# Kernel tuning notes

Hardware: AMD Instinct MI355X
Metric: run time of the kernel (lower is better)

Reference implementation:

```python
import jax, jax.numpy as jnp
import numpy as np

N, C_IN, C_OUT, H, W = 16, 256, 256, 32, 32
K = 9  # 3x3 kernel


def setup_inputs() -> dict:
    key = jax.random.key(0)
    k1, k2, k3 = jax.random.split(key, 3)
    x = jax.random.normal(k1, (N, C_IN, H, W), dtype=jnp.float32)
    # offsets as produced upstream from anchors: (N, H*W, 18)
    offset = jax.random.normal(k2, (N, H * W, 2 * K), dtype=jnp.float32)
    # DeformConv weight (no bias), kaiming-ish scale
    weight = jax.random.normal(k3, (C_OUT, C_IN, 3, 3), dtype=jnp.float32) * 0.02
    return {"x": x, "offset": offset, "weight": weight}


def _deform_conv3x3(x, offset_nchw, weight):
    """DeformConv v1, kernel 3x3, stride 1, padding 1, dilation 1,
    groups=1, deformable_groups=1, zero padding outside borders."""
    n, c, h, w = x.shape
    o = weight.shape[0]
    # offset channel layout: (dy_k, dx_k) pairs for k = 0..8
    off = offset_nchw.reshape(n, K, 2, h, w)
    dy = off[:, :, 0]  # (N,K,H,W)
    dx = off[:, :, 1]
    ky = (jnp.arange(K) // 3 - 1).astype(x.dtype)  # kernel row offsets -1,0,1
    kx = (jnp.arange(K) % 3 - 1).astype(x.dtype)
    base_y = jnp.arange(h, dtype=x.dtype)[None, None, :, None]
    base_x = jnp.arange(w, dtype=x.dtype)[None, None, None, :]
    py = base_y + ky[None, :, None, None] + dy  # (N,K,H,W) sample rows
    px = base_x + kx[None, :, None, None] + dx  # (N,K,H,W) sample cols

    y0 = jnp.floor(py)
    x0 = jnp.floor(px)
    ly = py - y0  # fractional parts
    lx = px - x0

    x_flat = x.reshape(n, c, h * w)

    def corner(yi, xi, wgt):
        valid = (yi >= 0) & (yi <= h - 1) & (xi >= 0) & (xi <= w - 1)
        yc = jnp.clip(yi, 0, h - 1).astype(jnp.int32)
        xc = jnp.clip(xi, 0, w - 1).astype(jnp.int32)
        idx = (yc * w + xc).reshape(n, K * h * w)
        g = jax.vmap(lambda xf, i: xf[:, i])(x_flat, idx)  # (N,C,K*H*W)
        wv = (wgt * valid.astype(x.dtype)).reshape(n, 1, K * h * w)
        return g * wv

    val = (corner(y0, x0, (1 - ly) * (1 - lx))
           + corner(y0, x0 + 1, (1 - ly) * lx)
           + corner(y0 + 1, x0, ly * (1 - lx))
           + corner(y0 + 1, x0 + 1, ly * lx))
    val = val.reshape(n, c, K, h, w)  # sampled im2col columns
    return jnp.einsum('nckhw,ock->nohw', val, weight.reshape(o, c, K))


def reference(x, offset, weight):
    n, _, h, w = x.shape
    assert h * w == offset.shape[1]
    # AdaptiveConv.forward: (N, HW, 18) -> (N, 18, H, W)
    offset_nchw = jnp.transpose(offset, (0, 2, 1)).reshape(n, 2 * K, h, w)
    return _deform_conv3x3(x, offset_nchw, weight)
```

## Files before the change

kernel.cpp:

```cpp
#include <hip/hip_runtime.h>

#define NB   16
#define CIN  256
#define COUT 256
#define HH   32
#define WW   32
#define HW   1024
#define KK   9
#define CK   2304

typedef __bf16 bf16x8 __attribute__((ext_vector_type(8)));
typedef float  f32x4  __attribute__((ext_vector_type(4)));

__device__ __forceinline__ unsigned short f2bf(float f) {
    unsigned int u = __float_as_uint(f);
    u += 0x7FFFu + ((u >> 16) & 1u);
    return (unsigned short)(u >> 16);
}
__device__ __forceinline__ float bfhi(unsigned int u) {
    return __uint_as_float(u & 0xFFFF0000u);
}
__device__ __forceinline__ float bflo(unsigned int u) {
    return __uint_as_float(u << 16);
}

typedef const __attribute__((address_space(1))) void* gas_ptr;
typedef __attribute__((address_space(3))) void* las_ptr;

__device__ __forceinline__ void async16(const void* g, void* l) {
    __builtin_amdgcn_global_load_lds((gas_ptr)g, (las_ptr)l, 16, 0, 0);
}

__global__ __launch_bounds__(256) void wconv_kernel(const float* __restrict__ w,
                                                    unsigned short* __restrict__ wbf) {
    __shared__ float ls[CK];
    const int o = blockIdx.x;
    const float* wo = w + (size_t)o * CK;
#pragma unroll
    for (int i = threadIdx.x; i < CK; i += 256) ls[i] = wo[i];
    __syncthreads();
    unsigned short* dst = wbf + (size_t)o * CK;
#pragma unroll
    for (int i = threadIdx.x; i < CK; i += 256) {
        int k = i >> 8, c = i & 255;
        dst[i] = f2bf(ls[c * KK + k]);
    }
}

__global__ __launch_bounds__(256) void xt_kernel(const float* __restrict__ x,
                                                 unsigned short* __restrict__ xtb) {
    __shared__ float ls[64][65];
    const int c0  = blockIdx.x * 64;
    const int hw0 = blockIdx.y * 64;
    const int n   = blockIdx.z;
    const int t   = threadIdx.x;
    {
        int c = t >> 2, q = t & 3;
        const float4* base = (const float4*)(x + ((size_t)(n * CIN + c0 + c)) * HW + hw0 + q * 16);
#pragma unroll
        for (int j = 0; j < 4; ++j) {
            float4 v = base[j];
            ls[c][q * 16 + j * 4 + 0] = v.x;
            ls[c][q * 16 + j * 4 + 1] = v.y;
            ls[c][q * 16 + j * 4 + 2] = v.z;
            ls[c][q * 16 + j * 4 + 3] = v.w;
        }
    }
    __syncthreads();
    {
        int hw = t >> 2, seg = (t & 3) * 16;
        unsigned int dw[8];
#pragma unroll
        for (int j = 0; j < 8; ++j) {
            float f0 = ls[seg + 2 * j][hw];
            float f1 = ls[seg + 2 * j + 1][hw];
            dw[j] = (unsigned)f2bf(f0) | ((unsigned)f2bf(f1) << 16);
        }
        uint4* dst = (uint4*)(xtb + ((size_t)(n * HW + hw0 + hw)) * CIN + c0 + seg);
        dst[0] = *(uint4*)&dw[0];
        dst[1] = *(uint4*)&dw[4];
    }
}

__global__ __launch_bounds__(512, 2) void fused_kernel(const unsigned short* __restrict__ wbf,
                                                       const unsigned short* __restrict__ xtb,
                                                       const float* __restrict__ off,
                                                       float* __restrict__ out) {
    __shared__ unsigned short As[2][256 * 64];
    __shared__ unsigned short Bs[2][64 * 64];

    const int tid  = threadIdx.x;
    const int wv   = tid >> 6;
    const int lane = tid & 63;
    const int quad = lane >> 4;
    const int l15  = lane & 15;

    const int hw_local = tid >> 3;
    const int seg      = tid & 7;

    const int id  = blockIdx.x;
    const int n   = ((id & 7) << 1) | ((id >> 3) & 1);
    const int hw0 = (id >> 4) * 64;

    const int hw = hw0 + hw_local;
    const int h  = hw >> 5, w = hw & 31;

    const int srow   = lane >> 3;
    const int schunk = (lane & 7) ^ (srow & 7);

    const uint4*  xb4  = (const uint4*)(xtb + (size_t)n * HW * CIN);
    const float2* offp = (const float2*)(off + ((size_t)n * HW + hw) * (2 * KK));

    f32x4 acc[2][4] = {};

    auto setup = [&](int tap, float wg[4], int ix[4]) {
        float2 o = offp[tap];
        float py = (float)(h + tap / 3 - 1) + o.x;
        float px = (float)(w + tap % 3 - 1) + o.y;
        float y0f = floorf(py), x0f = floorf(px);
        float ly = py - y0f, lx = px - x0f;
        int y0 = (int)y0f, x0 = (int)x0f;
#pragma unroll
        for (int c2 = 0; c2 < 4; ++c2) {
            int yy = y0 + (c2 >> 1);
            int xx = x0 + (c2 & 1);
            float wy = (c2 >> 1) ? ly : 1.0f - ly;
            float wx = (c2 & 1) ? lx : 1.0f - lx;
            bool v = (yy >= 0) && (yy < HH) && (xx >= 0) && (xx < WW);
            wg[c2] = v ? wy * wx : 0.0f;
            int yc = yy < 0 ? 0 : (yy > HH - 1 ? HH - 1 : yy);
            int xc = xx < 0 ? 0 : (xx > WW - 1 ? WW - 1 : xx);
            ix[c2] = yc * WW + xc;
        }
    };

    auto loadc = [&](uint4 cr[4], const int ix[4], int s) {
#pragma unroll
        for (int c2 = 0; c2 < 4; ++c2)
            cr[c2] = xb4[(size_t)ix[c2] * 32 + s * 8 + seg];
    };

    auto build = [&](int nb, int ckb, const uint4 cr[4], const float wg[4]) {
#pragma unroll
        for (int j = 0; j < 4; ++j) {
            int rb = wv * 32 + j * 8;
            async16(wbf + (size_t)(rb + srow) * CK + ckb + schunk * 8, &As[nb][rb * 64]);
        }
        unsigned u0[4], u1[4], u2[4], u3[4];
        *(uint4*)u0 = cr[0]; *(uint4*)u1 = cr[1];
        *(uint4*)u2 = cr[2]; *(uint4*)u3 = cr[3];
        unsigned dw[4];
#pragma unroll
        for (int d = 0; d < 4; ++d) {
            float lo = wg[0] * bflo(u0[d]) + wg[1] * bflo(u1[d])
                     + wg[2] * bflo(u2[d]) + wg[3] * bflo(u3[d]);
            float hi = wg[0] * bfhi(u0[d]) + wg[1] * bfhi(u1[d])
                     + wg[2] * bfhi(u2[d]) + wg[3] * bfhi(u3[d]);
            dw[d] = (unsigned)f2bf(lo) | ((unsigned)f2bf(hi) << 16);
        }
        *(uint4*)&Bs[nb][hw_local * 64 + (seg ^ (hw_local & 7)) * 8] = *(uint4*)dw;
    };

    auto mfma_step = [&](int pb) {
        bf16x8 af[2][2], bfr[4][2];
#pragma unroll
        for (int mi = 0; mi < 2; ++mi)
#pragma unroll
            for (int hh = 0; hh < 2; ++hh) {
                int row = wv * 32 + mi * 16 + l15;
                int ch  = (hh * 4 + quad) ^ (row & 7);
                af[mi][hh] = *(const bf16x8*)&As[pb][row * 64 + ch * 8];
            }
#pragma unroll
        for (int ni = 0; ni < 4; ++ni)
#pragma unroll
            for (int hh = 0; hh < 2; ++hh) {
                int row = ni * 16 + l15;
                int ch  = (hh * 4 + quad) ^ (row & 7);
                bfr[ni][hh] = *(const bf16x8*)&Bs[pb][row * 64 + ch * 8];
            }
#pragma unroll
        for (int mi = 0; mi < 2; ++mi)
#pragma unroll
            for (int ni = 0; ni < 4; ++ni) {
                acc[mi][ni] = __builtin_amdgcn_mfma_f32_16x16x32_bf16(af[mi][0], bfr[ni][0], acc[mi][ni], 0, 0, 0);
                acc[mi][ni] = __builtin_amdgcn_mfma_f32_16x16x32_bf16(af[mi][1], bfr[ni][1], acc[mi][ni], 0, 0, 0);
            }
    };

    float wgc[4], wgn[4];
    int   ixc[4], ixn[4];
    uint4 crA[4], crB[4];

    setup(0, wgc, ixc);
    loadc(crA, ixc, 0);
    build(0, 0, crA, wgc);
    loadc(crB, ixc, 1);
    __syncthreads();

    for (int tap = 0; tap < 9; ++tap) {
        const int ckb = tap * 256;
        build(1, ckb + 64, crB, wgc);
        loadc(crA, ixc, 2);
        mfma_step(0);
        __syncthreads();
        build(0, ckb + 128, crA, wgc);
        loadc(crB, ixc, 3);
        mfma_step(1);
        __syncthreads();
        build(1, ckb + 192, crB, wgc);
        if (tap < 8) { setup(tap + 1, wgn, ixn); loadc(crA, ixn, 0); }
        mfma_step(0);
        __syncthreads();
        if (tap < 8) {
            build(0, ckb + 256, crA, wgn);
            loadc(crB, ixn, 1);
#pragma unroll
            for (int c2 = 0; c2 < 4; ++c2) { wgc[c2] = wgn[c2]; ixc[c2] = ixn[c2]; }
            mfma_step(1);
            __syncthreads();
        } else {
            mfma_step(1);
        }
    }

    float* opnt = out + (size_t)n * COUT * HW + hw0;
#pragma unroll
    for (int mi = 0; mi < 2; ++mi)
#pragma unroll
        for (int ni = 0; ni < 4; ++ni) {
            int col = ni * 16 + l15;
#pragma unroll
            for (int rr = 0; rr < 4; ++rr) {
                int row = wv * 32 + mi * 16 + quad * 4 + rr;
                opnt[(size_t)row * HW + col] = acc[mi][ni][rr];
            }
        }
}

extern "C" void kernel_launch(void* const* d_in, const int* in_sizes, int n_in,
                              void* d_out, int out_size, void* d_ws, size_t ws_size,
                              hipStream_t stream) {
    const float* x   = (const float*)d_in[0];
    const float* off = (const float*)d_in[1];
    const float* wt  = (const float*)d_in[2];
    float* out = (float*)d_out;

    unsigned short* wbf = (unsigned short*)d_ws;
    unsigned short* xtb = (unsigned short*)((char*)d_ws + 1179648);

    wconv_kernel<<<256, 256, 0, stream>>>(wt, wbf);
    xt_kernel<<<dim3(4, 16, 16), 256, 0, stream>>>(x, xtb);
    fused_kernel<<<256, 512, 0, stream>>>(wbf, xtb, off, out);
}
```

Measured before the change: 122.3 us.

## Triple-buffer weight tiles with async LDS DMA and manual barrier scheduling

The weight (A) tile buffer goes from double to triple buffering, so each async global-to-LDS weight copy is issued two k-steps ahead instead of one. The original __syncthreads is replaced by a manual lgkmcnt wait plus s_barrier wrapped in sched_barriers, with explicit sched_barrier fences placed between the DMA, lerp, gather-load and MFMA phases. s_setprio is raised around the MFMA block. The aim is to hide weight-load latency and stop the compiler from reordering or over-waiting on memory. The third A buffer adds 32KB of LDS and the main loop is no longer unrolled. Waiting only on lgkmcnt could also let the async LDS loads (vmcnt) go unfinished before they are read.

Measured after the change: 122.1 us. About the same (-0.1%).

```diff
diff --git a/kernel.cpp b/kernel.cpp
--- a/kernel.cpp
+++ b/kernel.cpp
@@ -30,6 +30,10 @@
 __device__ __forceinline__ void async16(const void* g, void* l) {
     __builtin_amdgcn_global_load_lds((gas_ptr)g, (las_ptr)l, 16, 0, 0);
 }
+
+#define SB() __builtin_amdgcn_sched_barrier(0)
+#define SYNC() do { SB(); asm volatile("s_waitcnt lgkmcnt(0)" ::: "memory"); SB(); \
+                    __builtin_amdgcn_s_barrier(); SB(); } while (0)
 
 __global__ __launch_bounds__(256) void wconv_kernel(const float* __restrict__ w,
                                                     unsigned short* __restrict__ wbf) {
@@ -86,7 +90,7 @@
                                                        const unsigned short* __restrict__ xtb,
                                                        const float* __restrict__ off,
                                                        float* __restrict__ out) {
-    __shared__ unsigned short As[2][256 * 64];
+    __shared__ unsigned short As[3][256 * 64];
     __shared__ unsigned short Bs[2][64 * 64];
 
     const int tid  = threadIdx.x;
@@ -113,10 +117,9 @@
 
     f32x4 acc[2][4] = {};
 
-    auto setup = [&](int tap, float wg[4], int ix[4]) {
-        float2 o = offp[tap];
-        float py = (float)(h + tap / 3 - 1) + o.x;
-        float px = (float)(w + tap % 3 - 1) + o.y;
+    auto setup2 = [&](float2 o, int tapv, float* wg, int* ix) {
+        float py = (float)(h + tapv / 3 - 1) + o.x;
+        float px = (float)(w + tapv % 3 - 1) + o.y;
         float y0f = floorf(py), x0f = floorf(px);
         float ly = py - y0f, lx = px - x0f;
         int y0 = (int)y0f, x0 = (int)x0f;
@@ -134,18 +137,23 @@
         }
     };
 
-    auto loadc = [&](uint4 cr[4], const int ix[4], int s) {
+    auto loadc = [&](uint4 cr[4], const int* ix, int q) {
 #pragma unroll
         for (int c2 = 0; c2 < 4; ++c2)
-            cr[c2] = xb4[(size_t)ix[c2] * 32 + s * 8 + seg];
-    };
-
-    auto build = [&](int nb, int ckb, const uint4 cr[4], const float wg[4]) {
+            cr[c2] = xb4[(size_t)ix[c2] * 32 + q * 8 + seg];
+    };
+
+    auto dmaA = [&](int ai, int kblk) {
+        const unsigned short* wsrc = wbf + (size_t)kblk * 64 + (size_t)srow * CK + schunk * 8;
+        unsigned short* dst = &As[ai][0];
 #pragma unroll
         for (int j = 0; j < 4; ++j) {
             int rb = wv * 32 + j * 8;
-            async16(wbf + (size_t)(rb + srow) * CK + ckb + schunk * 8, &As[nb][rb * 64]);
-        }
+            async16(wsrc + (size_t)rb * CK, dst + rb * 64);
+        }
+    };
+
+    auto lerpB = [&](int bi, const uint4 cr[4], const float* wg) {
         unsigned u0[4], u1[4], u2[4], u3[4];
         *(uint4*)u0 = cr[0]; *(uint4*)u1 = cr[1];
         *(uint4*)u2 = cr[2]; *(uint4*)u3 = cr[3];
@@ -158,10 +166,12 @@
                      + wg[2] * bfhi(u2[d]) + wg[3] * bfhi(u3[d]);
             dw[d] = (unsigned)f2bf(lo) | ((unsigned)f2bf(hi) << 16);
         }
-        *(uint4*)&Bs[nb][hw_local * 64 + (seg ^ (hw_local & 7)) * 8] = *(uint4*)dw;
-    };
-
-    auto mfma_step = [&](int pb) {
+        *(uint4*)&Bs[bi][hw_local * 64 + (seg ^ (hw_local & 7)) * 8] = *(uint4*)dw;
+    };
+
+    auto mfma_step = [&](int ai, int bi) {
+        const unsigned short* Ap = &As[ai][0];
+        const unsigned short* Bp = &Bs[bi][0];
         bf16x8 af[2][2], bfr[4][2];
 #pragma unroll
         for (int mi = 0; mi < 2; ++mi)
@@ -169,7 +179,7 @@
             for (int hh = 0; hh < 2; ++hh) {
                 int row = wv * 32 + mi * 16 + l15;
                 int ch  = (hh * 4 + quad) ^ (row & 7);
-                af[mi][hh] = *(const bf16x8*)&As[pb][row * 64 + ch * 8];
+                af[mi][hh] = *(const bf16x8*)(Ap + row * 64 + ch * 8);
             }
 #pragma unroll
         for (int ni = 0; ni < 4; ++ni)
@@ -177,8 +187,9 @@
             for (int hh = 0; hh < 2; ++hh) {
                 int row = ni * 16 + l15;
                 int ch  = (hh * 4 + quad) ^ (row & 7);
-                bfr[ni][hh] = *(const bf16x8*)&Bs[pb][row * 64 + ch * 8];
+                bfr[ni][hh] = *(const bf16x8*)(Bp + row * 64 + ch * 8);
             }
+        __builtin_amdgcn_s_setprio(1);
 #pragma unroll
         for (int mi = 0; mi < 2; ++mi)
 #pragma unroll
@@ -186,42 +197,78 @@
                 acc[mi][ni] = __builtin_amdgcn_mfma_f32_16x16x32_bf16(af[mi][0], bfr[ni][0], acc[mi][ni], 0, 0, 0);
                 acc[mi][ni] = __builtin_amdgcn_mfma_f32_16x16x32_bf16(af[mi][1], bfr[ni][1], acc[mi][ni], 0, 0, 0);
             }
+        __builtin_amdgcn_s_setprio(0);
     };
 
     float wgc[4], wgn[4];
     int   ixc[4], ixn[4];
     uint4 crA[4], crB[4];
-
-    setup(0, wgc, ixc);
-    loadc(crA, ixc, 0);
-    build(0, 0, crA, wgc);
-    loadc(crB, ixc, 1);
-    __syncthreads();
-
+    {
+        float2 o0 = offp[0];
+        setup2(o0, 0, wgc, ixc);
+        dmaA(0, 0);
+        dmaA(1, 1);
+        SB();
+        loadc(crA, ixc, 0);
+        loadc(crB, ixc, 1);
+        SB();
+        lerpB(0, crA, wgc);
+        SYNC();
+    }
+
+    int i0 = 0;
+#pragma unroll 1
     for (int tap = 0; tap < 9; ++tap) {
-        const int ckb = tap * 256;
-        build(1, ckb + 64, crB, wgc);
+        const int i1 = (i0 == 2) ? 0 : i0 + 1;
+        const int i2 = (i1 == 2) ? 0 : i1 + 1;
+        const int kb = tap * 4;
+        const bool more = (tap < 8);
+
+        dmaA(i2, kb + 2);
+        SB();
+        lerpB(1, crB, wgc);
+        SB();
         loadc(crA, ixc, 2);
-        mfma_step(0);
-        __syncthreads();
-        build(0, ckb + 128, crA, wgc);
+        SB();
+        mfma_step(i0, 0);
+        SYNC();
+
+        dmaA(i0, kb + 3);
+        SB();
+        lerpB(0, crA, wgc);
+        SB();
         loadc(crB, ixc, 3);
-        mfma_step(1);
-        __syncthreads();
-        build(1, ckb + 192, crB, wgc);
-        if (tap < 8) { setup(tap + 1, wgn, ixn); loadc(crA, ixn, 0); }
-        mfma_step(0);
-        __syncthreads();
-        if (tap < 8) {
-            build(0, ckb + 256, crA, wgn);
+        SB();
+        mfma_step(i1, 1);
+        SYNC();
+
+        float2 onx = {};
+        if (more) onx = offp[tap + 1];
+        SB();
+        if (more) dmaA(i1, kb + 4);
+        SB();
+        lerpB(1, crB, wgc);
+        SB();
+        if (more) { setup2(onx, tap + 1, wgn, ixn); loadc(crA, ixn, 0); }
+        SB();
+        mfma_step(i2, 0);
+        SYNC();
+
+        if (more) {
+            dmaA(i2, kb + 5);
+            SB();
+            lerpB(0, crA, wgn);
+            SB();
             loadc(crB, ixn, 1);
 #pragma unroll
             for (int c2 = 0; c2 < 4; ++c2) { wgc[c2] = wgn[c2]; ixc[c2] = ixn[c2]; }
-            mfma_step(1);
-            __syncthreads();
+            SB();
+            mfma_step(i0, 1);
+            SYNC();
         } else {
-            mfma_step(1);
-        }
+            mfma_step(i0, 1);
+        }
+        i0 = i1;
     }
 
     float* opnt = out + (size_t)n * COUT * HW + hw0;
```
